# Optimization experiments

Hardware: AMD Instinct MI355X
Metric: run time of the kernel (lower is better)

The kernel has to match this reference:

```python
import jax, jax.numpy as jnp
import numpy as np

N_NODES = 50000
N_EDGES = 1_600_000
IN_CH = 256
HEADS = 4
OUT_CH = 32


def setup_inputs() -> dict:
    key = jax.random.key(0)
    k1, k2, k3, k4 = jax.random.split(key, 4)
    x = jax.random.normal(k1, (N_NODES, IN_CH), dtype=jnp.float32)
    edge_index = jax.random.randint(k2, (2, N_EDGES), 0, N_NODES, dtype=jnp.int32)
    # xavier-uniform-like init scales
    W = jax.random.uniform(k3, (IN_CH, HEADS * OUT_CH), dtype=jnp.float32,
                           minval=-1.0, maxval=1.0) * np.sqrt(6.0 / (IN_CH + HEADS * OUT_CH))
    attn = jax.random.uniform(k4, (HEADS, 2 * OUT_CH), dtype=jnp.float32,
                              minval=-1.0, maxval=1.0) * np.sqrt(6.0 / (HEADS + 2 * OUT_CH))
    return {"x": x, "edge_index": edge_index, "W": W, "attn": attn}


def reference(x, edge_index, W, attn):
    n = x.shape[0]
    H = attn.shape[0]
    C = attn.shape[1] // 2
    # h = lin(x).view(n, H, C)
    h = (x @ W).reshape(n, H, C)
    row, col = edge_index[0], edge_index[1]
    # (cat([h_row, h_col]) * attn).sum(-1) == h_row.a_src + h_col.a_dst;
    # compute per-node scores then gather per edge (cheaper, same math).
    a_src, a_dst = attn[:, :C], attn[:, C:]
    s_src = jnp.einsum('nhc,hc->nh', h, a_src)  # [n, H]
    s_dst = jnp.einsum('nhc,hc->nh', h, a_dst)  # [n, H]
    alpha = jax.nn.leaky_relu(s_src[row] + s_dst[col], 0.2)  # [E, H]
    # segment softmax over edges grouped by target node `row`
    seg_max = jax.ops.segment_max(alpha, row, num_segments=n)  # [n, H]
    ex = jnp.exp(alpha - seg_max[row])
    denom = jax.ops.segment_sum(ex, row, num_segments=n)  # [n, H]
    alpha_norm = ex / denom[row]  # [E, H]
    # weighted scatter-add of source features (dropout p=0.0 is identity)
    out = jax.ops.segment_sum(alpha_norm[..., None] * h[col], row, num_segments=n)  # [n,H,C]
    return out.mean(axis=1), alpha_norm
```

## Files before the change

kernel.cpp:

```cpp
#include <hip/hip_runtime.h>

#define NNODES 50000
#define NEDGES 1600000
#define IN_CH 256
#define HEADS 4
#define OUT_CH 32
#define HC 128
#define NSB ((NNODES + 255) / 256)
#define NCHUNK 128
#define CE 12500
#define WORDS 25000

typedef unsigned int u32;
typedef unsigned short u16;
typedef short bf16x8 __attribute__((ext_vector_type(8)));
typedef u16 u16x8 __attribute__((ext_vector_type(8)));
typedef float f32x4 __attribute__((ext_vector_type(4)));

__device__ __forceinline__ float b2f(u16 s) { return __uint_as_float(((u32)s) << 16); }
__device__ __forceinline__ u16 f2b(float f) {
  u32 u = __float_as_uint(f);
  u32 r = (u + 0x7FFFu + ((u >> 16) & 1u)) >> 16;
  return (u16)r;
}
__device__ __forceinline__ float lrelu(float v) { return v >= 0.f ? v : 0.2f * v; }

__global__ __launch_bounds__(256) void k_wprep(const float* __restrict__ W,
                                               u16* __restrict__ wt) {
  int i = blockIdx.x * 256 + threadIdx.x;
  if (i >= IN_CH * HC) return;
  int kk = i & 31;
  int n = (i >> 5) & 127;
  int kt = i >> 12;
  wt[i] = f2b(W[(size_t)(kt * 32 + kk) * HC + n]);
}

__global__ __launch_bounds__(256) void k_gemm(const float* __restrict__ x,
                                              const u16* __restrict__ wt,
                                              const float* __restrict__ attn,
                                              u16* __restrict__ hb,
                                              float* __restrict__ s_src,
                                              float* __restrict__ s_dst) {
  __shared__ union {
    struct {
      u16 xh[64 * 32];
      u16 xl[64 * 32];
      u16 wh[128 * 32];
    } st;
    float cbuf[64 * 132];
  } L;
  __shared__ float sA[256];
  const int tid = threadIdx.x;
  const int wave = tid >> 6;
  const int lane = tid & 63;
  const int row0 = blockIdx.x * 64;
  sA[tid] = attn[tid];

  f32x4 acc[4][2] = {};
  const int frow = lane & 15;
  const int koff = (lane >> 4) << 4;

  const int sr = tid >> 2;
  const int skc = (tid & 3) << 3;
  const int sgrow = row0 + sr;
  const int sxb = (sr << 6) + (skc << 1);
  const int sxs = sxb ^ ((sr & 7) << 4);

  for (int kt = 0; kt < 8; ++kt) {
    {
      float4 v0 = make_float4(0.f, 0.f, 0.f, 0.f), v1 = v0;
      if (sgrow < NNODES) {
        const float* px = &x[(size_t)sgrow * IN_CH + kt * 32 + skc];
        v0 = *(const float4*)px;
        v1 = *(const float4*)(px + 4);
      }
      float vv[8] = {v0.x, v0.y, v0.z, v0.w, v1.x, v1.y, v1.z, v1.w};
      u16x8 hi, lo;
#pragma unroll
      for (int i = 0; i < 8; ++i) {
        u16 h = f2b(vv[i]);
        hi[i] = h;
        lo[i] = f2b(vv[i] - b2f(h));
      }
      *(u16x8*)((char*)L.st.xh + sxs) = hi;
      *(u16x8*)((char*)L.st.xl + sxs) = lo;
    }
#pragma unroll
    for (int li = 0; li < 2; ++li) {
      int i = tid + (li << 8);
      int col = i >> 2;
      int kb = (i & 3) << 4;
      u16x8 v = *(const u16x8*)((const char*)wt + (((size_t)(kt * 128 + col)) << 6) + kb);
      int sb = ((col << 6) + kb) ^ ((col & 7) << 4);
      *(u16x8*)((char*)L.st.wh + sb) = v;
    }
    __syncthreads();
    bf16x8 ah[4], al[4], bw[2];
#pragma unroll
    for (int mi = 0; mi < 4; ++mi) {
      int r = mi * 16 + frow;
      int sb = ((r << 6) + koff) ^ ((r & 7) << 4);
      ah[mi] = *(bf16x8*)((char*)L.st.xh + sb);
      al[mi] = *(bf16x8*)((char*)L.st.xl + sb);
    }
#pragma unroll
    for (int ni = 0; ni < 2; ++ni) {
      int c = (wave << 5) + ni * 16 + frow;
      int sb = ((c << 6) + koff) ^ ((c & 7) << 4);
      bw[ni] = *(bf16x8*)((char*)L.st.wh + sb);
    }
#pragma unroll
    for (int mi = 0; mi < 4; ++mi)
#pragma unroll
      for (int ni = 0; ni < 2; ++ni) {
        acc[mi][ni] = __builtin_amdgcn_mfma_f32_16x16x32_bf16(ah[mi], bw[ni], acc[mi][ni], 0, 0, 0);
        acc[mi][ni] = __builtin_amdgcn_mfma_f32_16x16x32_bf16(al[mi], bw[ni], acc[mi][ni], 0, 0, 0);
      }
    __syncthreads();
  }

#pragma unroll
  for (int mi = 0; mi < 4; ++mi)
#pragma unroll
    for (int ni = 0; ni < 2; ++ni) {
#pragma unroll
      for (int reg = 0; reg < 4; ++reg) {
        int row = mi * 16 + ((lane >> 4) << 2) + reg;
        int col = (wave << 5) + (ni << 4) + frow;
        L.cbuf[row * 132 + col] = acc[mi][ni][reg];
      }
    }
  __syncthreads();

  const int tc = tid & 31;
  const int tr = tid >> 5;
  const int head = tc >> 3;
  const int cb = (tc & 7) << 2;
  const float4 as4 = *(const float4*)&sA[head * 64 + cb];
  const float4 ad4 = *(const float4*)&sA[head * 64 + 32 + cb];
#pragma unroll
  for (int i = 0; i < 8; ++i) {
    int row = (tr << 3) + i;
    int grow = row0 + row;
    float4 v = *(const float4*)&L.cbuf[row * 132 + (tc << 2)];
    float ps = v.x * as4.x + v.y * as4.y + v.z * as4.z + v.w * as4.w;
    float pd = v.x * ad4.x + v.y * ad4.y + v.z * ad4.z + v.w * ad4.w;
    ps += __shfl_xor(ps, 1); ps += __shfl_xor(ps, 2); ps += __shfl_xor(ps, 4);
    pd += __shfl_xor(pd, 1); pd += __shfl_xor(pd, 2); pd += __shfl_xor(pd, 4);
    if (grow < NNODES) {
      u16 q[4] = {f2b(v.x), f2b(v.y), f2b(v.z), f2b(v.w)};
      *(ushort4*)&hb[(size_t)grow * HC + (tc << 2)] = *(ushort4*)q;
      if ((tc & 7) == 0) {
        s_src[(size_t)grow * 4 + head] = ps;
        s_dst[(size_t)grow * 4 + head] = pd;
      }
    }
  }
}

__global__ __launch_bounds__(256) void k_chist(const int* __restrict__ rowi,
                                               u32* __restrict__ chunk_hist,
                                               u16* __restrict__ lslot) {
  __shared__ u32 lh[WORDS];
  const int c = blockIdx.x;
  const int tid = threadIdx.x;
  for (int i = tid; i < WORDS; i += 256) lh[i] = 0;
  __syncthreads();
  const int base = c * CE;
  for (int i = tid; i < CE; i += 256) {
    int e = base + i;
    int r = rowi[e];
    u32 sh = (u32)(r & 1) << 4;
    u32 old = atomicAdd(&lh[r >> 1], 1u << sh);
    lslot[e] = (u16)((old >> sh) & 0xFFFFu);
  }
  __syncthreads();
  u32* dst = chunk_hist + (size_t)c * WORDS;
  for (int i = tid; i < WORDS; i += 256) dst[i] = lh[i];
}

__global__ __launch_bounds__(256) void k_cscan(u32* __restrict__ chunk_hist,
                                               int* __restrict__ counts) {
  __shared__ u32 tile[NCHUNK][64];
  const int w0 = blockIdx.x * 64;
  const int tid = threadIdx.x;
  for (int i = tid; i < NCHUNK * 64; i += 256) {
    int c = i >> 6, wl = i & 63;
    int w = w0 + wl;
    tile[c][wl] = (w < WORDS) ? chunk_hist[(size_t)c * WORDS + w] : 0u;
  }
  __syncthreads();
  if (tid < 64) {
    u32 slo = 0, shi = 0;
    for (int c = 0; c < NCHUNK; ++c) {
      u32 v = tile[c][tid];
      tile[c][tid] = slo | (shi << 16);
      slo += v & 0xFFFFu;
      shi += v >> 16;
    }
    int w = w0 + tid;
    if (w < WORDS) {
      int r = w << 1;
      if (r < NNODES) counts[r] = (int)slo;
      if (r + 1 < NNODES) counts[r + 1] = (int)shi;
    }
  }
  __syncthreads();
  for (int i = tid; i < NCHUNK * 64; i += 256) {
    int c = i >> 6, wl = i & 63;
    int w = w0 + wl;
    if (w < WORDS) chunk_hist[(size_t)c * WORDS + w] = tile[c][wl];
  }
}

__global__ __launch_bounds__(256) void k_scan1(const int* __restrict__ counts,
                                               int* __restrict__ bsum) {
  int i = blockIdx.x * 256 + threadIdx.x;
  int v = (i < NNODES) ? counts[i] : 0;
#pragma unroll
  for (int m = 1; m < 64; m <<= 1) v += __shfl_xor(v, m);
  __shared__ int ws[4];
  if ((threadIdx.x & 63) == 0) ws[threadIdx.x >> 6] = v;
  __syncthreads();
  if (threadIdx.x == 0) bsum[blockIdx.x] = ws[0] + ws[1] + ws[2] + ws[3];
}

__global__ __launch_bounds__(256) void k_scan2(const int* __restrict__ bsum,
                                               int* __restrict__ boff) {
  __shared__ int s[256];
  int t = threadIdx.x;
  int v = (t < NSB) ? bsum[t] : 0;
  s[t] = v;
  __syncthreads();
  for (int off = 1; off < 256; off <<= 1) {
    int u = (t >= off) ? s[t - off] : 0;
    __syncthreads();
    s[t] += u;
    __syncthreads();
  }
  boff[t] = s[t] - v;
}

__global__ __launch_bounds__(256) void k_scan3(const int* __restrict__ counts,
                                               const int* __restrict__ boff,
                                               int* __restrict__ row_ptr) {
  __shared__ int s[256];
  int t = threadIdx.x;
  int i = blockIdx.x * 256 + t;
  int v = (i < NNODES) ? counts[i] : 0;
  s[t] = v;
  __syncthreads();
  for (int off = 1; off < 256; off <<= 1) {
    int u = (t >= off) ? s[t - off] : 0;
    __syncthreads();
    s[t] += u;
    __syncthreads();
  }
  if (i < NNODES) row_ptr[i] = boff[blockIdx.x] + s[t] - v;
  if (i == 0) row_ptr[NNODES] = NEDGES;
}

__global__ void k_scatter(const int* __restrict__ rowi, const int* __restrict__ coli,
                          const int* __restrict__ row_ptr,
                          const u32* __restrict__ chunk_hist,
                          const u16* __restrict__ lslot,
                          int* __restrict__ col_csr) {
  int e = blockIdx.x * 256 + threadIdx.x;
  if (e >= NEDGES) return;
  int r = rowi[e];
  int c = e / CE;
  u32 word = chunk_hist[(size_t)c * WORDS + (r >> 1)];
  int off = (int)((word >> ((u32)(r & 1) << 4)) & 0xFFFFu);
  int pos = row_ptr[r] + off + (int)lslot[e];
  col_csr[pos] = coli[e];
}

__global__ __launch_bounds__(256) void k_softmax(const int* __restrict__ col_csr,
                                                 const int* __restrict__ row_ptr,
                                                 const float* __restrict__ s_src,
                                                 const float* __restrict__ s_dst,
                                                 float* __restrict__ mx_out,
                                                 float* __restrict__ rden_out,
                                                 u16* __restrict__ an16) {
  const int wid = threadIdx.x >> 6;
  const int lane = threadIdx.x & 63;
  const int r = blockIdx.x * 4 + wid;
  if (r >= NNODES) return;
  const int p0 = row_ptr[r], p1 = row_ptr[r + 1];
  const int deg = p1 - p0;
  if (deg == 0) return;
  const float4 ss = *(const float4*)&s_src[(size_t)r * 4];
  const float NEG = -3.0e38f;

  if (deg <= 64) {
    float4 al = make_float4(NEG, NEG, NEG, NEG);
    if (lane < deg) {
      int c = col_csr[p0 + lane];
      float4 sd = *(const float4*)&s_dst[(size_t)c * 4];
      al.x = lrelu(ss.x + sd.x);
      al.y = lrelu(ss.y + sd.y);
      al.z = lrelu(ss.z + sd.z);
      al.w = lrelu(ss.w + sd.w);
    }
    float4 mx = al;
#pragma unroll
    for (int m = 1; m < 64; m <<= 1) {
      mx.x = fmaxf(mx.x, __shfl_xor(mx.x, m));
      mx.y = fmaxf(mx.y, __shfl_xor(mx.y, m));
      mx.z = fmaxf(mx.z, __shfl_xor(mx.z, m));
      mx.w = fmaxf(mx.w, __shfl_xor(mx.w, m));
    }
    float4 ex = make_float4(0.f, 0.f, 0.f, 0.f);
    if (lane < deg) {
      ex.x = __expf(al.x - mx.x);
      ex.y = __expf(al.y - mx.y);
      ex.z = __expf(al.z - mx.z);
      ex.w = __expf(al.w - mx.w);
    }
    float4 sm = ex;
#pragma unroll
    for (int m = 1; m < 64; m <<= 1) {
      sm.x += __shfl_xor(sm.x, m);
      sm.y += __shfl_xor(sm.y, m);
      sm.z += __shfl_xor(sm.z, m);
      sm.w += __shfl_xor(sm.w, m);
    }
    float4 rd = make_float4(1.f / sm.x, 1.f / sm.y, 1.f / sm.z, 1.f / sm.w);
    if (lane == 0) {
      *(float4*)&mx_out[(size_t)r * 4] = mx;
      *(float4*)&rden_out[(size_t)r * 4] = rd;
    }
    if (lane < deg) {
      u16 q[4] = {f2b(ex.x * rd.x), f2b(ex.y * rd.y), f2b(ex.z * rd.z), f2b(ex.w * rd.w)};
      *(ushort4*)&an16[(size_t)(p0 + lane) * 4] = *(ushort4*)q;
    }
  } else {
    float4 mx = make_float4(NEG, NEG, NEG, NEG);
    for (int p = p0 + lane; p < p1; p += 64) {
      int c = col_csr[p];
      float4 sd = *(const float4*)&s_dst[(size_t)c * 4];
      mx.x = fmaxf(mx.x, lrelu(ss.x + sd.x));
      mx.y = fmaxf(mx.y, lrelu(ss.y + sd.y));
      mx.z = fmaxf(mx.z, lrelu(ss.z + sd.z));
      mx.w = fmaxf(mx.w, lrelu(ss.w + sd.w));
    }
#pragma unroll
    for (int m = 1; m < 64; m <<= 1) {
      mx.x = fmaxf(mx.x, __shfl_xor(mx.x, m));
      mx.y = fmaxf(mx.y, __shfl_xor(mx.y, m));
      mx.z = fmaxf(mx.z, __shfl_xor(mx.z, m));
      mx.w = fmaxf(mx.w, __shfl_xor(mx.w, m));
    }
    float4 sm = make_float4(0.f, 0.f, 0.f, 0.f);
    for (int p = p0 + lane; p < p1; p += 64) {
      int c = col_csr[p];
      float4 sd = *(const float4*)&s_dst[(size_t)c * 4];
      sm.x += __expf(lrelu(ss.x + sd.x) - mx.x);
      sm.y += __expf(lrelu(ss.y + sd.y) - mx.y);
      sm.z += __expf(lrelu(ss.z + sd.z) - mx.z);
      sm.w += __expf(lrelu(ss.w + sd.w) - mx.w);
    }
#pragma unroll
    for (int m = 1; m < 64; m <<= 1) {
      sm.x += __shfl_xor(sm.x, m);
      sm.y += __shfl_xor(sm.y, m);
      sm.z += __shfl_xor(sm.z, m);
      sm.w += __shfl_xor(sm.w, m);
    }
    float4 rd = make_float4(1.f / sm.x, 1.f / sm.y, 1.f / sm.z, 1.f / sm.w);
    if (lane == 0) {
      *(float4*)&mx_out[(size_t)r * 4] = mx;
      *(float4*)&rden_out[(size_t)r * 4] = rd;
    }
    for (int p = p0 + lane; p < p1; p += 64) {
      int c = col_csr[p];
      float4 sd = *(const float4*)&s_dst[(size_t)c * 4];
      float4 ex;
      ex.x = __expf(lrelu(ss.x + sd.x) - mx.x);
      ex.y = __expf(lrelu(ss.y + sd.y) - mx.y);
      ex.z = __expf(lrelu(ss.z + sd.z) - mx.z);
      ex.w = __expf(lrelu(ss.w + sd.w) - mx.w);
      u16 q[4] = {f2b(ex.x * rd.x), f2b(ex.y * rd.y), f2b(ex.z * rd.z), f2b(ex.w * rd.w)};
      *(ushort4*)&an16[(size_t)p * 4] = *(ushort4*)q;
    }
  }
}

__global__ void k_alphaf(const int* __restrict__ rowi, const int* __restrict__ coli,
                         const float* __restrict__ s_src, const float* __restrict__ s_dst,
                         const float* __restrict__ mx, const float* __restrict__ rden,
                         float* __restrict__ alpha_out) {
  int e = blockIdx.x * 256 + threadIdx.x;
  if (e >= NEDGES) return;
  int r = rowi[e], c = coli[e];
  float4 ss = *(const float4*)&s_src[(size_t)r * 4];
  float4 sd = *(const float4*)&s_dst[(size_t)c * 4];
  float4 m4 = *(const float4*)&mx[(size_t)r * 4];
  float4 rd = *(const float4*)&rden[(size_t)r * 4];
  float4 an;
  an.x = __expf(lrelu(ss.x + sd.x) - m4.x) * rd.x;
  an.y = __expf(lrelu(ss.y + sd.y) - m4.y) * rd.y;
  an.z = __expf(lrelu(ss.z + sd.z) - m4.z) * rd.z;
  an.w = __expf(lrelu(ss.w + sd.w) - m4.w) * rd.w;
  *(float4*)&alpha_out[(size_t)e * 4] = an;
}

__global__ __launch_bounds__(256) void k_aggr(const int* __restrict__ col_csr,
                                              const int* __restrict__ row_ptr,
                                              const u16* __restrict__ an16,
                                              const u16* __restrict__ hb,
                                              float* __restrict__ out_mean) {
  const int wid = threadIdx.x >> 6;
  const int lane = threadIdx.x & 63;
  const int r = blockIdx.x * 4 + wid;
  if (r >= NNODES) return;
  const int p0 = row_ptr[r], p1 = row_ptr[r + 1];
  const int hd = lane >> 4;
  const int ch = lane << 1;
  float acc0 = 0.f, acc1 = 0.f;

  int p = p0;
  for (; p + 8 <= p1; p += 8) {
    int cs[8];
    float ws[8];
    u32 hv[8];
#pragma unroll
    for (int i = 0; i < 8; ++i) cs[i] = col_csr[p + i];
#pragma unroll
    for (int i = 0; i < 8; ++i) ws[i] = b2f(an16[(size_t)(p + i) * 4 + hd]);
#pragma unroll
    for (int i = 0; i < 8; ++i) hv[i] = *(const u32*)&hb[(size_t)cs[i] * HC + ch];
#pragma unroll
    for (int i = 0; i < 8; ++i) {
      acc0 += ws[i] * b2f((u16)(hv[i] & 0xFFFFu));
      acc1 += ws[i] * b2f((u16)(hv[i] >> 16));
    }
  }
  for (; p < p1; ++p) {
    int c = col_csr[p];
    float w = b2f(an16[(size_t)p * 4 + hd]);
    u32 hv = *(const u32*)&hb[(size_t)c * HC + ch];
    acc0 += w * b2f((u16)(hv & 0xFFFFu));
    acc1 += w * b2f((u16)(hv >> 16));
  }
  acc0 += __shfl_xor(acc0, 16);
  acc0 += __shfl_xor(acc0, 32);
  acc1 += __shfl_xor(acc1, 16);
  acc1 += __shfl_xor(acc1, 32);
  if (lane < 16) {
    float2 o = make_float2(acc0 * 0.25f, acc1 * 0.25f);
    *(float2*)&out_mean[(size_t)r * 32 + (lane << 1)] = o;
  }
}

extern "C" void kernel_launch(void* const* d_in, const int* in_sizes, int n_in,
                              void* d_out, int out_size, void* d_ws, size_t ws_size,
                              hipStream_t stream) {
  const float* x = (const float*)d_in[0];
  const int* ei = (const int*)d_in[1];
  const float* W = (const float*)d_in[2];
  const float* attn = (const float*)d_in[3];
  const int* rowi = ei;
  const int* coli = ei + NEDGES;

  float* out_mean = (float*)d_out;
  float* alpha_out = (float*)d_out + (size_t)NNODES * 32;

  char* w = (char*)d_ws;
  u16* hb = (u16*)w;          w += (size_t)NNODES * HC * 2;
  u16* an16 = (u16*)w;        w += (size_t)NEDGES * 4 * 2;
  float* s_src = (float*)w;   w += (size_t)NNODES * 4 * 4;
  float* s_dst = (float*)w;   w += (size_t)NNODES * 4 * 4;
  float* mx = (float*)w;      w += (size_t)NNODES * 4 * 4;
  float* rden = (float*)w;    w += (size_t)NNODES * 4 * 4;
  int* counts = (int*)w;      w += (size_t)NNODES * 4;
  int* bsum = (int*)w;        w += (size_t)256 * 4;
  int* boff = (int*)w;        w += (size_t)256 * 4;
  int* row_ptr = (int*)w;     w += (size_t)50016 * 4;
  u16* lslot = (u16*)w;       w += (size_t)NEDGES * 2;
  int* col_csr = (int*)w;     w += (size_t)NEDGES * 4;
  u32* chunk_hist = (u32*)w;  w += (size_t)NCHUNK * WORDS * 4;
  u16* wt = (u16*)w;          w += (size_t)IN_CH * HC * 2;

  k_wprep<<<(IN_CH * HC + 255) / 256, 256, 0, stream>>>(W, wt);
  k_gemm<<<(NNODES + 63) / 64, 256, 0, stream>>>(x, wt, attn, hb, s_src, s_dst);
  k_chist<<<NCHUNK, 256, 0, stream>>>(rowi, chunk_hist, lslot);
  k_cscan<<<(WORDS + 63) / 64, 256, 0, stream>>>(chunk_hist, counts);
  k_scan1<<<NSB, 256, 0, stream>>>(counts, bsum);
  k_scan2<<<1, 256, 0, stream>>>(bsum, boff);
  k_scan3<<<NSB, 256, 0, stream>>>(counts, boff, row_ptr);
  k_scatter<<<(NEDGES + 255) / 256, 256, 0, stream>>>(rowi, coli, row_ptr, chunk_hist, lslot, col_csr);
  k_softmax<<<(NNODES + 3) / 4, 256, 0, stream>>>(col_csr, row_ptr, s_src, s_dst, mx, rden, an16);
  k_alphaf<<<(NEDGES + 255) / 256, 256, 0, stream>>>(rowi, coli, s_src, s_dst, mx, rden, alpha_out);
  k_aggr<<<(NNODES + 3) / 4, 256, 0, stream>>>(col_csr, row_ptr, an16, hb, out_mean);
}
```

Measured before the change: 231.4 us.

## Fuse segment softmax and weighted aggregation into one per-row kernel

Result: no change. 236.0 us (+2.0%).

```diff
diff --git a/kernel.cpp b/kernel.cpp
--- a/kernel.cpp
+++ b/kernel.cpp
@@ -275,27 +275,38 @@
   col_csr[pos] = coli[e];
 }
 
-__global__ __launch_bounds__(256) void k_softmax(const int* __restrict__ col_csr,
-                                                 const int* __restrict__ row_ptr,
-                                                 const float* __restrict__ s_src,
-                                                 const float* __restrict__ s_dst,
-                                                 float* __restrict__ mx_out,
-                                                 float* __restrict__ rden_out,
-                                                 u16* __restrict__ an16) {
+__global__ __launch_bounds__(256) void k_rowfused(const int* __restrict__ col_csr,
+                                                  const int* __restrict__ row_ptr,
+                                                  const float* __restrict__ s_src,
+                                                  const float* __restrict__ s_dst,
+                                                  const u16* __restrict__ hb,
+                                                  float* __restrict__ mx_out,
+                                                  float* __restrict__ rden_out,
+                                                  float* __restrict__ out_mean) {
   const int wid = threadIdx.x >> 6;
   const int lane = threadIdx.x & 63;
   const int r = blockIdx.x * 4 + wid;
   if (r >= NNODES) return;
   const int p0 = row_ptr[r], p1 = row_ptr[r + 1];
   const int deg = p1 - p0;
-  if (deg == 0) return;
+  const int hd = lane >> 4;
+  const int ch = lane << 1;
+  if (deg == 0) {
+    if (lane < 16) {
+      float2 z = make_float2(0.f, 0.f);
+      *(float2*)&out_mean[(size_t)r * 32 + (lane << 1)] = z;
+    }
+    return;
+  }
   const float4 ss = *(const float4*)&s_src[(size_t)r * 4];
   const float NEG = -3.0e38f;
+  float acc0 = 0.f, acc1 = 0.f;
 
   if (deg <= 64) {
+    int c = 0;
     float4 al = make_float4(NEG, NEG, NEG, NEG);
     if (lane < deg) {
-      int c = col_csr[p0 + lane];
+      c = col_csr[p0 + lane];
       float4 sd = *(const float4*)&s_dst[(size_t)c * 4];
       al.x = lrelu(ss.x + sd.x);
       al.y = lrelu(ss.y + sd.y);
@@ -330,19 +341,41 @@
       *(float4*)&mx_out[(size_t)r * 4] = mx;
       *(float4*)&rden_out[(size_t)r * 4] = rd;
     }
-    if (lane < deg) {
-      u16 q[4] = {f2b(ex.x * rd.x), f2b(ex.y * rd.y), f2b(ex.z * rd.z), f2b(ex.w * rd.w)};
-      *(ushort4*)&an16[(size_t)(p0 + lane) * 4] = *(ushort4*)q;
+    int w01 = (int)(((u32)f2b(ex.x * rd.x)) | ((u32)f2b(ex.y * rd.y) << 16));
+    int w23 = (int)(((u32)f2b(ex.z * rd.z)) | ((u32)f2b(ex.w * rd.w) << 16));
+    const int nblk = (deg + 7) >> 3;
+    for (int b = 0; b < nblk; ++b) {
+      const int i0 = b << 3;
+      u32 hv[8];
+      float wv[8];
+#pragma unroll
+      for (int j = 0; j < 8; ++j) {
+        int cj = __shfl(c, i0 + j);
+        u32 u01 = (u32)__shfl(w01, i0 + j);
+        u32 u23 = (u32)__shfl(w23, i0 + j);
+        u32 us = (hd < 2) ? u01 : u23;
+        u16 wb = (hd & 1) ? (u16)(us >> 16) : (u16)(us & 0xFFFFu);
+        wv[j] = b2f(wb);
+        hv[j] = *(const u32*)&hb[(size_t)cj * HC + ch];
+      }
+#pragma unroll
+      for (int j = 0; j < 8; ++j) {
+        acc0 += wv[j] * b2f((u16)(hv[j] & 0xFFFFu));
+        acc1 += wv[j] * b2f((u16)(hv[j] >> 16));
+      }
     }
   } else {
     float4 mx = make_float4(NEG, NEG, NEG, NEG);
-    for (int p = p0 + lane; p < p1; p += 64) {
-      int c = col_csr[p];
-      float4 sd = *(const float4*)&s_dst[(size_t)c * 4];
-      mx.x = fmaxf(mx.x, lrelu(ss.x + sd.x));
-      mx.y = fmaxf(mx.y, lrelu(ss.y + sd.y));
-      mx.z = fmaxf(mx.z, lrelu(ss.z + sd.z));
-      mx.w = fmaxf(mx.w, lrelu(ss.w + sd.w));
+    for (int base = p0; base < p1; base += 64) {
+      int idx = base + lane;
+      if (idx < p1) {
+        int c = col_csr[idx];
+        float4 sd = *(const float4*)&s_dst[(size_t)c * 4];
+        mx.x = fmaxf(mx.x, lrelu(ss.x + sd.x));
+        mx.y = fmaxf(mx.y, lrelu(ss.y + sd.y));
+        mx.z = fmaxf(mx.z, lrelu(ss.z + sd.z));
+        mx.w = fmaxf(mx.w, lrelu(ss.w + sd.w));
+      }
     }
 #pragma unroll
     for (int m = 1; m < 64; m <<= 1) {
@@ -352,13 +385,16 @@
       mx.w = fmaxf(mx.w, __shfl_xor(mx.w, m));
     }
     float4 sm = make_float4(0.f, 0.f, 0.f, 0.f);
-    for (int p = p0 + lane; p < p1; p += 64) {
-      int c = col_csr[p];
-      float4 sd = *(const float4*)&s_dst[(size_t)c * 4];
-      sm.x += __expf(lrelu(ss.x + sd.x) - mx.x);
-      sm.y += __expf(lrelu(ss.y + sd.y) - mx.y);
-      sm.z += __expf(lrelu(ss.z + sd.z) - mx.z);
-      sm.w += __expf(lrelu(ss.w + sd.w) - mx.w);
+    for (int base = p0; base < p1; base += 64) {
+      int idx = base + lane;
+      if (idx < p1) {
+        int c = col_csr[idx];
+        float4 sd = *(const float4*)&s_dst[(size_t)c * 4];
+        sm.x += __expf(lrelu(ss.x + sd.x) - mx.x);
+        sm.y += __expf(lrelu(ss.y + sd.y) - mx.y);
+        sm.z += __expf(lrelu(ss.z + sd.z) - mx.z);
+        sm.w += __expf(lrelu(ss.w + sd.w) - mx.w);
+      }
     }
 #pragma unroll
     for (int m = 1; m < 64; m <<= 1) {
@@ -372,17 +408,52 @@
       *(float4*)&mx_out[(size_t)r * 4] = mx;
       *(float4*)&rden_out[(size_t)r * 4] = rd;
     }
-    for (int p = p0 + lane; p < p1; p += 64) {
-      int c = col_csr[p];
-      float4 sd = *(const float4*)&s_dst[(size_t)c * 4];
-      float4 ex;
-      ex.x = __expf(lrelu(ss.x + sd.x) - mx.x);
-      ex.y = __expf(lrelu(ss.y + sd.y) - mx.y);
-      ex.z = __expf(lrelu(ss.z + sd.z) - mx.z);
-      ex.w = __expf(lrelu(ss.w + sd.w) - mx.w);
-      u16 q[4] = {f2b(ex.x * rd.x), f2b(ex.y * rd.y), f2b(ex.z * rd.z), f2b(ex.w * rd.w)};
-      *(ushort4*)&an16[(size_t)p * 4] = *(ushort4*)q;
-    }
+    for (int base = p0; base < p1; base += 64) {
+      int idx = base + lane;
+      int c = 0;
+      float4 ex = make_float4(0.f, 0.f, 0.f, 0.f);
+      if (idx < p1) {
+        c = col_csr[idx];
+        float4 sd = *(const float4*)&s_dst[(size_t)c * 4];
+        ex.x = __expf(lrelu(ss.x + sd.x) - mx.x) * rd.x;
+        ex.y = __expf(lrelu(ss.y + sd.y) - mx.y) * rd.y;
+        ex.z = __expf(lrelu(ss.z + sd.z) - mx.z) * rd.z;
+        ex.w = __expf(lrelu(ss.w + sd.w) - mx.w) * rd.w;
+      }
+      int w01 = (int)(((u32)f2b(ex.x)) | ((u32)f2b(ex.y) << 16));
+      int w23 = (int)(((u32)f2b(ex.z)) | ((u32)f2b(ex.w) << 16));
+      int cnt = min(64, p1 - base);
+      const int nblk = (cnt + 7) >> 3;
+      for (int b = 0; b < nblk; ++b) {
+        const int i0 = b << 3;
+        u32 hv[8];
+        float wv[8];
+#pragma unroll
+        for (int j = 0; j < 8; ++j) {
+          int cj = __shfl(c, i0 + j);
+          u32 u01 = (u32)__shfl(w01, i0 + j);
+          u32 u23 = (u32)__shfl(w23, i0 + j);
+          u32 us = (hd < 2) ? u01 : u23;
+          u16 wb = (hd & 1) ? (u16)(us >> 16) : (u16)(us & 0xFFFFu);
+          wv[j] = b2f(wb);
+          hv[j] = *(const u32*)&hb[(size_t)cj * HC + ch];
+        }
+#pragma unroll
+        for (int j = 0; j < 8; ++j) {
+          acc0 += wv[j] * b2f((u16)(hv[j] & 0xFFFFu));
+          acc1 += wv[j] * b2f((u16)(hv[j] >> 16));
+        }
+      }
+    }
+  }
+
+  acc0 += __shfl_xor(acc0, 16);
+  acc0 += __shfl_xor(acc0, 32);
+  acc1 += __shfl_xor(acc1, 16);
+  acc1 += __shfl_xor(acc1, 32);
+  if (lane < 16) {
+    float2 o = make_float2(acc0 * 0.25f, acc1 * 0.25f);
+    *(float2*)&out_mean[(size_t)r * 32 + (lane << 1)] = o;
   }
 }
 
@@ -405,54 +476,6 @@
   *(float4*)&alpha_out[(size_t)e * 4] = an;
 }
 
-__global__ __launch_bounds__(256) void k_aggr(const int* __restrict__ col_csr,
-                                              const int* __restrict__ row_ptr,
-                                              const u16* __restrict__ an16,
-                                              const u16* __restrict__ hb,
-                                              float* __restrict__ out_mean) {
-  const int wid = threadIdx.x >> 6;
-  const int lane = threadIdx.x & 63;
-  const int r = blockIdx.x * 4 + wid;
-  if (r >= NNODES) return;
-  const int p0 = row_ptr[r], p1 = row_ptr[r + 1];
-  const int hd = lane >> 4;
-  const int ch = lane << 1;
-  float acc0 = 0.f, acc1 = 0.f;
-
-  int p = p0;
-  for (; p + 8 <= p1; p += 8) {
-    int cs[8];
-    float ws[8];
-    u32 hv[8];
-#pragma unroll
-    for (int i = 0; i < 8; ++i) cs[i] = col_csr[p + i];
-#pragma unroll
-    for (int i = 0; i < 8; ++i) ws[i] = b2f(an16[(size_t)(p + i) * 4 + hd]);
-#pragma unroll
-    for (int i = 0; i < 8; ++i) hv[i] = *(const u32*)&hb[(size_t)cs[i] * HC + ch];
-#pragma unroll
-    for (int i = 0; i < 8; ++i) {
-      acc0 += ws[i] * b2f((u16)(hv[i] & 0xFFFFu));
-      acc1 += ws[i] * b2f((u16)(hv[i] >> 16));
-    }
-  }
-  for (; p < p1; ++p) {
-    int c = col_csr[p];
-    float w = b2f(an16[(size_t)p * 4 + hd]);
-    u32 hv = *(const u32*)&hb[(size_t)c * HC + ch];
-    acc0 += w * b2f((u16)(hv & 0xFFFFu));
-    acc1 += w * b2f((u16)(hv >> 16));
-  }
-  acc0 += __shfl_xor(acc0, 16);
-  acc0 += __shfl_xor(acc0, 32);
-  acc1 += __shfl_xor(acc1, 16);
-  acc1 += __shfl_xor(acc1, 32);
-  if (lane < 16) {
-    float2 o = make_float2(acc0 * 0.25f, acc1 * 0.25f);
-    *(float2*)&out_mean[(size_t)r * 32 + (lane << 1)] = o;
-  }
-}
-
 extern "C" void kernel_launch(void* const* d_in, const int* in_sizes, int n_in,
                               void* d_out, int out_size, void* d_ws, size_t ws_size,
                               hipStream_t stream) {
@@ -468,7 +491,6 @@
 
   char* w = (char*)d_ws;
   u16* hb = (u16*)w;          w += (size_t)NNODES * HC * 2;
-  u16* an16 = (u16*)w;        w += (size_t)NEDGES * 4 * 2;
   float* s_src = (float*)w;   w += (size_t)NNODES * 4 * 4;
   float* s_dst = (float*)w;   w += (size_t)NNODES * 4 * 4;
   float* mx = (float*)w;      w += (size_t)NNODES * 4 * 4;
@@ -490,7 +512,6 @@
   k_scan2<<<1, 256, 0, stream>>>(bsum, boff);
   k_scan3<<<NSB, 256, 0, stream>>>(counts, boff, row_ptr);
   k_scatter<<<(NEDGES + 255) / 256, 256, 0, stream>>>(rowi, coli, row_ptr, chunk_hist, lslot, col_csr);
-  k_softmax<<<(NNODES + 3) / 4, 256, 0, stream>>>(col_csr, row_ptr, s_src, s_dst, mx, rden, an16);
+  k_rowfused<<<(NNODES + 3) / 4, 256, 0, stream>>>(col_csr, row_ptr, s_src, s_dst, hb, mx, rden, out_mean);
   k_alphaf<<<(NEDGES + 255) / 256, 256, 0, stream>>>(rowi, coli, s_src, s_dst, mx, rden, alpha_out);
-  k_aggr<<<(NNODES + 3) / 4, 256, 0, stream>>>(col_csr, row_ptr, an16, hb, out_mean);
-}
+}
```

## Fuse alpha output into softmax via edge-id CSR and widen aggregation lanes

Applied to the files above, without the earlier changes.

New measurement: 232.5 us. About the same (+0.5%).

```diff
diff --git a/kernel.cpp b/kernel.cpp
--- a/kernel.cpp
+++ b/kernel.cpp
@@ -264,7 +264,7 @@
                           const int* __restrict__ row_ptr,
                           const u32* __restrict__ chunk_hist,
                           const u16* __restrict__ lslot,
-                          int* __restrict__ col_csr) {
+                          int* __restrict__ col_csr, int* __restrict__ eid_csr) {
   int e = blockIdx.x * 256 + threadIdx.x;
   if (e >= NEDGES) return;
   int r = rowi[e];
@@ -273,14 +273,15 @@
   int off = (int)((word >> ((u32)(r & 1) << 4)) & 0xFFFFu);
   int pos = row_ptr[r] + off + (int)lslot[e];
   col_csr[pos] = coli[e];
+  eid_csr[pos] = e;
 }
 
 __global__ __launch_bounds__(256) void k_softmax(const int* __restrict__ col_csr,
+                                                 const int* __restrict__ eid_csr,
                                                  const int* __restrict__ row_ptr,
                                                  const float* __restrict__ s_src,
                                                  const float* __restrict__ s_dst,
-                                                 float* __restrict__ mx_out,
-                                                 float* __restrict__ rden_out,
+                                                 float* __restrict__ alpha_out,
                                                  u16* __restrict__ an16) {
   const int wid = threadIdx.x >> 6;
   const int lane = threadIdx.x & 63;
@@ -293,9 +294,11 @@
   const float NEG = -3.0e38f;
 
   if (deg <= 64) {
+    int e = 0;
     float4 al = make_float4(NEG, NEG, NEG, NEG);
     if (lane < deg) {
       int c = col_csr[p0 + lane];
+      e = eid_csr[p0 + lane];
       float4 sd = *(const float4*)&s_dst[(size_t)c * 4];
       al.x = lrelu(ss.x + sd.x);
       al.y = lrelu(ss.y + sd.y);
@@ -325,13 +328,10 @@
       sm.z += __shfl_xor(sm.z, m);
       sm.w += __shfl_xor(sm.w, m);
     }
-    float4 rd = make_float4(1.f / sm.x, 1.f / sm.y, 1.f / sm.z, 1.f / sm.w);
-    if (lane == 0) {
-      *(float4*)&mx_out[(size_t)r * 4] = mx;
-      *(float4*)&rden_out[(size_t)r * 4] = rd;
-    }
     if (lane < deg) {
-      u16 q[4] = {f2b(ex.x * rd.x), f2b(ex.y * rd.y), f2b(ex.z * rd.z), f2b(ex.w * rd.w)};
+      float4 an = make_float4(ex.x / sm.x, ex.y / sm.y, ex.z / sm.z, ex.w / sm.w);
+      *(float4*)&alpha_out[(size_t)e * 4] = an;
+      u16 q[4] = {f2b(an.x), f2b(an.y), f2b(an.z), f2b(an.w)};
       *(ushort4*)&an16[(size_t)(p0 + lane) * 4] = *(ushort4*)q;
     }
   } else {
@@ -368,41 +368,20 @@
       sm.w += __shfl_xor(sm.w, m);
     }
     float4 rd = make_float4(1.f / sm.x, 1.f / sm.y, 1.f / sm.z, 1.f / sm.w);
-    if (lane == 0) {
-      *(float4*)&mx_out[(size_t)r * 4] = mx;
-      *(float4*)&rden_out[(size_t)r * 4] = rd;
-    }
     for (int p = p0 + lane; p < p1; p += 64) {
       int c = col_csr[p];
+      int e = eid_csr[p];
       float4 sd = *(const float4*)&s_dst[(size_t)c * 4];
-      float4 ex;
-      ex.x = __expf(lrelu(ss.x + sd.x) - mx.x);
-      ex.y = __expf(lrelu(ss.y + sd.y) - mx.y);
-      ex.z = __expf(lrelu(ss.z + sd.z) - mx.z);
-      ex.w = __expf(lrelu(ss.w + sd.w) - mx.w);
-      u16 q[4] = {f2b(ex.x * rd.x), f2b(ex.y * rd.y), f2b(ex.z * rd.z), f2b(ex.w * rd.w)};
+      float4 an;
+      an.x = __expf(lrelu(ss.x + sd.x) - mx.x) * rd.x;
+      an.y = __expf(lrelu(ss.y + sd.y) - mx.y) * rd.y;
+      an.z = __expf(lrelu(ss.z + sd.z) - mx.z) * rd.z;
+      an.w = __expf(lrelu(ss.w + sd.w) - mx.w) * rd.w;
+      *(float4*)&alpha_out[(size_t)e * 4] = an;
+      u16 q[4] = {f2b(an.x), f2b(an.y), f2b(an.z), f2b(an.w)};
       *(ushort4*)&an16[(size_t)p * 4] = *(ushort4*)q;
     }
   }
-}
-
-__global__ void k_alphaf(const int* __restrict__ rowi, const int* __restrict__ coli,
-                         const float* __restrict__ s_src, const float* __restrict__ s_dst,
-                         const float* __restrict__ mx, const float* __restrict__ rden,
-                         float* __restrict__ alpha_out) {
-  int e = blockIdx.x * 256 + threadIdx.x;
-  if (e >= NEDGES) return;
-  int r = rowi[e], c = coli[e];
-  float4 ss = *(const float4*)&s_src[(size_t)r * 4];
-  float4 sd = *(const float4*)&s_dst[(size_t)c * 4];
-  float4 m4 = *(const float4*)&mx[(size_t)r * 4];
-  float4 rd = *(const float4*)&rden[(size_t)r * 4];
-  float4 an;
-  an.x = __expf(lrelu(ss.x + sd.x) - m4.x) * rd.x;
-  an.y = __expf(lrelu(ss.y + sd.y) - m4.y) * rd.y;
-  an.z = __expf(lrelu(ss.z + sd.z) - m4.z) * rd.z;
-  an.w = __expf(lrelu(ss.w + sd.w) - m4.w) * rd.w;
-  *(float4*)&alpha_out[(size_t)e * 4] = an;
 }
 
 __global__ __launch_bounds__(256) void k_aggr(const int* __restrict__ col_csr,
@@ -415,41 +394,58 @@
   const int r = blockIdx.x * 4 + wid;
   if (r >= NNODES) return;
   const int p0 = row_ptr[r], p1 = row_ptr[r + 1];
-  const int hd = lane >> 4;
-  const int ch = lane << 1;
-  float acc0 = 0.f, acc1 = 0.f;
+  const int half = lane >> 5;
+  const int sl = lane & 31;
+  const int hd = sl >> 3;
+  const int boff = sl << 3;
+  float a0 = 0.f, a1 = 0.f, a2 = 0.f, a3 = 0.f;
 
   int p = p0;
-  for (; p + 8 <= p1; p += 8) {
+  for (; p + 16 <= p1; p += 16) {
     int cs[8];
-    float ws[8];
-    u32 hv[8];
-#pragma unroll
-    for (int i = 0; i < 8; ++i) cs[i] = col_csr[p + i];
-#pragma unroll
-    for (int i = 0; i < 8; ++i) ws[i] = b2f(an16[(size_t)(p + i) * 4 + hd]);
-#pragma unroll
-    for (int i = 0; i < 8; ++i) hv[i] = *(const u32*)&hb[(size_t)cs[i] * HC + ch];
+    float wv[8];
+    u32 h0[8], h1[8];
 #pragma unroll
     for (int i = 0; i < 8; ++i) {
-      acc0 += ws[i] * b2f((u16)(hv[i] & 0xFFFFu));
-      acc1 += ws[i] * b2f((u16)(hv[i] >> 16));
-    }
-  }
-  for (; p < p1; ++p) {
-    int c = col_csr[p];
-    float w = b2f(an16[(size_t)p * 4 + hd]);
-    u32 hv = *(const u32*)&hb[(size_t)c * HC + ch];
-    acc0 += w * b2f((u16)(hv & 0xFFFFu));
-    acc1 += w * b2f((u16)(hv >> 16));
-  }
-  acc0 += __shfl_xor(acc0, 16);
-  acc0 += __shfl_xor(acc0, 32);
-  acc1 += __shfl_xor(acc1, 16);
-  acc1 += __shfl_xor(acc1, 32);
-  if (lane < 16) {
-    float2 o = make_float2(acc0 * 0.25f, acc1 * 0.25f);
-    *(float2*)&out_mean[(size_t)r * 32 + (lane << 1)] = o;
+      int idx = p + (i << 1) + half;
+      cs[i] = col_csr[idx];
+      wv[i] = b2f(an16[(size_t)idx * 4 + hd]);
+    }
+#pragma unroll
+    for (int i = 0; i < 8; ++i) {
+      const u32* hp = (const u32*)((const char*)hb + ((size_t)cs[i] << 8) + boff);
+      h0[i] = hp[0];
+      h1[i] = hp[1];
+    }
+#pragma unroll
+    for (int i = 0; i < 8; ++i) {
+      a0 += wv[i] * __uint_as_float(h0[i] << 16);
+      a1 += wv[i] * __uint_as_float(h0[i] & 0xFFFF0000u);
+      a2 += wv[i] * __uint_as_float(h1[i] << 16);
+      a3 += wv[i] * __uint_as_float(h1[i] & 0xFFFF0000u);
+    }
+  }
+  for (; p < p1; p += 2) {
+    int idx = p + half;
+    bool act = idx < p1;
+    int c = act ? col_csr[idx] : 0;
+    float w = act ? b2f(an16[(size_t)idx * 4 + hd]) : 0.f;
+    const u32* hp = (const u32*)((const char*)hb + ((size_t)c << 8) + boff);
+    u32 x0 = hp[0], x1 = hp[1];
+    a0 += w * __uint_as_float(x0 << 16);
+    a1 += w * __uint_as_float(x0 & 0xFFFF0000u);
+    a2 += w * __uint_as_float(x1 << 16);
+    a3 += w * __uint_as_float(x1 & 0xFFFF0000u);
+  }
+  a0 += __shfl_xor(a0, 32); a1 += __shfl_xor(a1, 32);
+  a2 += __shfl_xor(a2, 32); a3 += __shfl_xor(a3, 32);
+  a0 += __shfl_xor(a0, 8);  a1 += __shfl_xor(a1, 8);
+  a2 += __shfl_xor(a2, 8);  a3 += __shfl_xor(a3, 8);
+  a0 += __shfl_xor(a0, 16); a1 += __shfl_xor(a1, 16);
+  a2 += __shfl_xor(a2, 16); a3 += __shfl_xor(a3, 16);
+  if (lane < 8) {
+    float4 o = make_float4(a0 * 0.25f, a1 * 0.25f, a2 * 0.25f, a3 * 0.25f);
+    *(float4*)&out_mean[(size_t)r * 32 + (lane << 2)] = o;
   }
 }
 
@@ -471,14 +467,13 @@
   u16* an16 = (u16*)w;        w += (size_t)NEDGES * 4 * 2;
   float* s_src = (float*)w;   w += (size_t)NNODES * 4 * 4;
   float* s_dst = (float*)w;   w += (size_t)NNODES * 4 * 4;
-  float* mx = (float*)w;      w += (size_t)NNODES * 4 * 4;
-  float* rden = (float*)w;    w += (size_t)NNODES * 4 * 4;
   int* counts = (int*)w;      w += (size_t)NNODES * 4;
   int* bsum = (int*)w;        w += (size_t)256 * 4;
   int* boff = (int*)w;        w += (size_t)256 * 4;
   int* row_ptr = (int*)w;     w += (size_t)50016 * 4;
   u16* lslot = (u16*)w;       w += (size_t)NEDGES * 2;
   int* col_csr = (int*)w;     w += (size_t)NEDGES * 4;
+  int* eid_csr = (int*)w;     w += (size_t)NEDGES * 4;
   u32* chunk_hist = (u32*)w;  w += (size_t)NCHUNK * WORDS * 4;
   u16* wt = (u16*)w;          w += (size_t)IN_CH * HC * 2;
 
@@ -489,8 +484,7 @@
   k_scan1<<<NSB, 256, 0, stream>>>(counts, bsum);
   k_scan2<<<1, 256, 0, stream>>>(bsum, boff);
   k_scan3<<<NSB, 256, 0, stream>>>(counts, boff, row_ptr);
-  k_scatter<<<(NEDGES + 255) / 256, 256, 0, stream>>>(rowi, coli, row_ptr, chunk_hist, lslot, col_csr);
-  k_softmax<<<(NNODES + 3) / 4, 256, 0, stream>>>(col_csr, row_ptr, s_src, s_dst, mx, rden, an16);
-  k_alphaf<<<(NEDGES + 255) / 256, 256, 0, stream>>>(rowi, coli, s_src, s_dst, mx, rden, alpha_out);
+  k_scatter<<<(NEDGES + 255) / 256, 256, 0, stream>>>(rowi, coli, row_ptr, chunk_hist, lslot, col_csr, eid_csr);
+  k_softmax<<<(NNODES + 3) / 4, 256, 0, stream>>>(col_csr, eid_csr, row_ptr, s_src, s_dst, alpha_out, an16);
   k_aggr<<<(NNODES + 3) / 4, 256, 0, stream>>>(col_csr, row_ptr, an16, hb, out_mean);
 }
```
